# Kernel tuning notes

Measured on AMD Instinct MI355X. Metric: run time of the kernel, lower is better.

Reference implementation:

```python
import jax, jax.numpy as jnp
import numpy as np


def setup_inputs() -> dict:
    key = jax.random.key(0)
    k1, k2 = jax.random.split(key)
    B, C, H, W = 8, 64, 128, 512
    image_tensor = jax.random.normal(k1, (B, C, H, W), dtype=jnp.float32)
    # positive metric depths in ~[1, 56] m
    depth = jax.random.uniform(k2, (B, H, W), dtype=jnp.float32) * 55.0 + 1.0
    fx = fy = 500.0; cx = 512.0; cy = 128.0  # intrinsics for original 1024x256 image
    camera_k = jnp.tile(jnp.array([[fx, 0.0, cx], [0.0, fy, cy], [0.0, 0.0, 1.0]],
                                  dtype=jnp.float32)[None], (B, 1, 1))
    meter_per_pixel = jnp.full((1,), 0.25, dtype=jnp.float32)
    return {"image_tensor": image_tensor, "camera_k": camera_k, "depth": depth,
            "meter_per_pixel": meter_per_pixel, "sat_width": 512,
            "ori_grdH": 256, "ori_grdW": 1024}


def reference(image_tensor, camera_k, depth, meter_per_pixel, sat_width, ori_grdH, ori_grdW):
    B, C, H, W = image_tensor.shape
    half = sat_width // 2
    mpp = meter_per_pixel.reshape(())

    # scale intrinsics from original image size to feature-map size (rows 0 and 1)
    row_scale = jnp.array([W / ori_grdW, H / ori_grdH, 1.0], dtype=jnp.float32)
    ck = camera_k * row_scale[None, :, None]
    k_inv = jnp.linalg.inv(ck)  # [B,3,3]

    # back-project pixel grid: xyz_w[b,h,w,:] = K^-1 @ [u,v,1]
    v, u = jnp.meshgrid(jnp.arange(H, dtype=jnp.float32),
                        jnp.arange(W, dtype=jnp.float32), indexing='ij')
    uv1 = jnp.stack([u, v, jnp.ones_like(u)], axis=-1)          # [H,W,3]
    xyz_w = jnp.einsum('bij,hwj->bhwi', k_inv, uv1)             # [B,H,W,3]
    # depth is already at (H,W): bilinear same-size resize is identity
    xyz = (xyz_w * depth[..., None] * 1.2).reshape(B * H * W, 3)

    feats = image_tensor.transpose(0, 2, 3, 1).reshape(B * H * W, C)

    # voxelize x,z (torch .long() truncates toward zero)
    x = jnp.trunc(xyz[:, 0] / mpp).astype(jnp.int32)
    z = jnp.trunc(xyz[:, 2] / mpp).astype(jnp.int32)
    y = xyz[:, 1]
    b = jnp.repeat(jnp.arange(B, dtype=jnp.int32), H * W)

    kept = (x >= -half) & (x <= half - 1) & (z >= -half) & (z <= half - 1)
    max_h = jnp.max(jnp.where(kept, y, -jnp.inf))
    xx = x + half
    zz = z + half
    h = max_h - y  # height key; the last entry per voxel (max h) survives dedup

    # voxel rank (same encoding as torch); out-of-bounds points get a sentinel
    rank0 = zz * (sat_width * B) + (xx + 1) * B + b
    SENT = sat_width * sat_width * B + B
    rank0 = jnp.where(kept, rank0, SENT)

    # torch: sort by h, then stable sort by rank0  == lexsort(primary=rank0, secondary=h)
    order = jnp.lexsort((h, rank0))
    r_s = rank0[order]
    f_s = feats[order]
    b_s, xx_s, zz_s = b[order], xx[order], zz[order]

    # keep the last point of each rank0 group (highest h in that voxel)
    is_last = jnp.concatenate([r_s[:-1] != r_s[1:], jnp.array([True])])
    valid = is_last & (r_s != SENT)

    flat = b_s * (sat_width * sat_width) + xx_s * sat_width + zz_s
    flat = jnp.where(valid, flat, B * sat_width * sat_width)  # invalid -> OOB, dropped

    final = jnp.zeros((B * sat_width * sat_width, C), dtype=jnp.float32)
    final = final.at[flat].set(f_s, mode='drop')
    return final.reshape(B, sat_width, sat_width, C).transpose(0, 3, 1, 2)
```

## Files before the change

### kernel.cpp

```cpp
#include <hip/hip_runtime.h>

#define BB 8
#define CC 64
#define HH 128
#define WW 512
#define SS 512
#define HALF 256
#define HWP (HH * WW)
#define BHW (BB * HWP)
#define CELLS (BB * SS * SS)

__device__ __forceinline__ unsigned int order_f32(float f) {
    unsigned int u = __float_as_uint(f);
    return (u & 0x80000000u) ? ~u : (u | 0x80000000u);
}

__global__ __launch_bounds__(256) void proj_kernel(
    const float* __restrict__ camera_k,
    const float* __restrict__ depth,
    const float* __restrict__ mpp_p,
    unsigned long long* __restrict__ keys)
{
    __shared__ float sk[9];
    const int idx = blockIdx.x * 256 + threadIdx.x;
    const int b = idx >> 16;

    if (threadIdx.x == 0) {
        const float rs[3] = {0.5f, 0.5f, 1.0f};
        double a[9];
        #pragma unroll
        for (int i = 0; i < 3; ++i)
            #pragma unroll
            for (int j = 0; j < 3; ++j)
                a[i*3 + j] = (double)__fmul_rn(camera_k[b*9 + i*3 + j], rs[i]);
        double det = a[0]*(a[4]*a[8]-a[5]*a[7])
                   - a[1]*(a[3]*a[8]-a[5]*a[6])
                   + a[2]*(a[3]*a[7]-a[4]*a[6]);
        double inv[9];
        inv[0] =  (a[4]*a[8]-a[5]*a[7])/det;
        inv[1] = -(a[1]*a[8]-a[2]*a[7])/det;
        inv[2] =  (a[1]*a[5]-a[2]*a[4])/det;
        inv[3] = -(a[3]*a[8]-a[5]*a[6])/det;
        inv[4] =  (a[0]*a[8]-a[2]*a[6])/det;
        inv[5] = -(a[0]*a[5]-a[2]*a[3])/det;
        inv[6] =  (a[3]*a[7]-a[4]*a[6])/det;
        inv[7] = -(a[0]*a[7]-a[1]*a[6])/det;
        inv[8] =  (a[0]*a[4]-a[1]*a[3])/det;
        #pragma unroll
        for (int i = 0; i < 9; ++i) sk[i] = (float)inv[i];
    }
    __syncthreads();

    const int rem = idx & (HWP - 1);
    const int v = rem >> 9;
    const int u = rem & (WW - 1);
    const float d = depth[idx];
    const float mpp = mpp_p[0];
    const float uf = (float)u, vf = (float)v;

    float xw = __fadd_rn(__fadd_rn(__fmul_rn(sk[0], uf), __fmul_rn(sk[1], vf)), sk[2]);
    float yw = __fadd_rn(__fadd_rn(__fmul_rn(sk[3], uf), __fmul_rn(sk[4], vf)), sk[5]);
    float zw = __fadd_rn(__fadd_rn(__fmul_rn(sk[6], uf), __fmul_rn(sk[7], vf)), sk[8]);
    float x3 = __fmul_rn(__fmul_rn(xw, d), 1.2f);
    float y3 = __fmul_rn(__fmul_rn(yw, d), 1.2f);
    float z3 = __fmul_rn(__fmul_rn(zw, d), 1.2f);

    int xi = (int)truncf(__fdiv_rn(x3, mpp));
    int zi = (int)truncf(__fdiv_rn(z3, mpp));

    if (xi >= -HALF && xi <= HALF - 1 && zi >= -HALF && zi <= HALF - 1) {
        int cell = (b << 18) | ((xi + HALF) << 9) | (zi + HALF);
        unsigned long long key =
            ((unsigned long long)order_f32(y3) << 32) | (unsigned int)(~idx);
        atomicMin(&keys[cell], key);
    }
}

__global__ __launch_bounds__(256) void scatter_kernel(
    const float* __restrict__ img,
    const unsigned long long* __restrict__ keys,
    float* __restrict__ out)
{
    const int cidx = blockIdx.x * 256 + threadIdx.x;
    const unsigned long long key = keys[cidx];
    const bool has = (key != ~0ull);
    const unsigned int pix = ~(unsigned int)(key & 0xFFFFFFFFull);
    const int b = cidx >> 18;
    const int rem = (int)(pix & (HWP - 1));

    const float* src = img + ((size_t)b * CC) * HWP + rem;
    const size_t obase = ((size_t)b * CC) * (size_t)(SS * SS) + (size_t)(cidx & (SS * SS - 1));

    #pragma unroll 16
    for (int c = 0; c < CC; ++c) {
        float val = 0.0f;
        if (has) val = src[(size_t)c * HWP];
        out[obase + (size_t)c * (SS * SS)] = val;
    }
}

extern "C" void kernel_launch(void* const* d_in, const int* in_sizes, int n_in,
                              void* d_out, int out_size, void* d_ws, size_t ws_size,
                              hipStream_t stream) {
    const float* img      = (const float*)d_in[0];
    const float* camera_k = (const float*)d_in[1];
    const float* depth    = (const float*)d_in[2];
    const float* mpp      = (const float*)d_in[3];

    unsigned long long* keys = (unsigned long long*)d_ws;

    hipMemsetAsync(keys, 0xFF, (size_t)CELLS * sizeof(unsigned long long), stream);

    proj_kernel<<<BHW / 256, 256, 0, stream>>>(camera_k, depth, mpp, keys);
    scatter_kernel<<<CELLS / 256, 256, 0, stream>>>(img, keys, (float*)d_out);
}
```

Before: 860.3 us.

## Restructure scatter kernel: 4 cells per thread, 4-channel slices, float4 stores

```diff
diff --git a/kernel.cpp b/kernel.cpp
--- a/kernel.cpp
+++ b/kernel.cpp
@@ -81,21 +81,40 @@
     const unsigned long long* __restrict__ keys,
     float* __restrict__ out)
 {
-    const int cidx = blockIdx.x * 256 + threadIdx.x;
-    const unsigned long long key = keys[cidx];
-    const bool has = (key != ~0ull);
-    const unsigned int pix = ~(unsigned int)(key & 0xFFFFFFFFull);
-    const int b = cidx >> 18;
-    const int rem = (int)(pix & (HWP - 1));
+    const int q     = blockIdx.x * 256 + threadIdx.x;
+    const int c0    = blockIdx.y << 2;
+    const int cell0 = q << 2;
+    const int b     = cell0 >> 18;
+    const int local = cell0 & (SS * SS - 1);
 
-    const float* src = img + ((size_t)b * CC) * HWP + rem;
-    const size_t obase = ((size_t)b * CC) * (size_t)(SS * SS) + (size_t)(cidx & (SS * SS - 1));
+    const ulonglong2* kp = (const ulonglong2*)keys + (size_t)q * 2;
+    const ulonglong2 ka = kp[0];
+    const ulonglong2 kb = kp[1];
+    const unsigned long long k[4] = {ka.x, ka.y, kb.x, kb.y};
 
-    #pragma unroll 16
-    for (int c = 0; c < CC; ++c) {
-        float val = 0.0f;
-        if (has) val = src[(size_t)c * HWP];
-        out[obase + (size_t)c * (SS * SS)] = val;
+    int  rem[4];
+    bool has[4];
+    #pragma unroll
+    for (int i = 0; i < 4; ++i) {
+        has[i] = (k[i] != ~0ull);
+        rem[i] = (int)((~(unsigned int)(k[i] & 0xFFFFFFFFull)) & (HWP - 1));
+    }
+
+    const float* plane0 = img + ((size_t)(b * CC + c0)) * HWP;
+    float*       op     = out + ((size_t)(b * CC + c0)) * (size_t)(SS * SS) + local;
+
+    float v[4][4];
+    #pragma unroll
+    for (int c = 0; c < 4; ++c) {
+        const float* pl = plane0 + (size_t)c * HWP;
+        #pragma unroll
+        for (int i = 0; i < 4; ++i)
+            v[c][i] = has[i] ? pl[rem[i]] : 0.0f;
+    }
+    #pragma unroll
+    for (int c = 0; c < 4; ++c) {
+        float4 f4 = make_float4(v[c][0], v[c][1], v[c][2], v[c][3]);
+        *(float4*)(op + (size_t)c * (SS * SS)) = f4;
     }
 }
 
@@ -112,5 +131,7 @@
     hipMemsetAsync(keys, 0xFF, (size_t)CELLS * sizeof(unsigned long long), stream);
 
     proj_kernel<<<BHW / 256, 256, 0, stream>>>(camera_k, depth, mpp, keys);
-    scatter_kernel<<<CELLS / 256, 256, 0, stream>>>(img, keys, (float*)d_out);
+
+    dim3 sgrid(CELLS / 4 / 256, CC / 4);
+    scatter_kernel<<<sgrid, 256, 0, stream>>>(img, keys, (float*)d_out);
 }
```

Result: faster. 796.5 us (-7.4%).
